# Kernel tuning notes

Hardware: AMD Instinct MI355X
Metric: run time of the kernel (lower is better)

The kernel has to match this reference:

```python
import jax, jax.numpy as jnp
import numpy as np

T, H, I, E, K = 8192, 2048, 768, 16, 2  # tokens, hidden, moe_intermediate, experts, top_k


def setup_inputs() -> dict:
    key = jax.random.key(0)
    k0, k1, k2, k3, k4 = jax.random.split(key, 5)
    return {
        "hidden_states": jax.random.normal(k0, (T, H), jnp.float32),
        "top_k_index": jax.random.randint(k1, (T, K), 0, E),
        "top_k_weights": jax.random.uniform(k2, (T, K), jnp.float32),
        "gate_up_proj": jax.random.normal(k3, (E, 2 * I, H), jnp.float32) * 0.02,
        "down_proj": jax.random.normal(k4, (E, H, I), jnp.float32) * 0.02,
    }


def reference(hidden_states, top_k_index, top_k_weights, gate_up_proj, down_proj):
    num_experts = gate_up_proj.shape[0]
    # combine[t, e] = sum over k of top_k_weights[t, k] where top_k_index[t, k] == e
    # (duplicated expert picks sum their weights, matching torch index_add_ semantics)
    onehot = jax.nn.one_hot(top_k_index, num_experts, dtype=hidden_states.dtype)  # [T, K, E]
    combine = jnp.einsum("tke,tk->te", onehot, top_k_weights)                      # [T, E]
    out = jnp.zeros_like(hidden_states)
    # fixed small loop over structurally distinct experts; unselected tokens get weight 0
    for e in range(num_experts):
        gate_up = hidden_states @ gate_up_proj[e].T        # [T, 2I]
        gate, up = jnp.split(gate_up, 2, axis=-1)
        act = jax.nn.silu(gate) * up                       # SwiGLU, [T, I]
        down = act @ down_proj[e].T                        # [T, H]
        out = out + down * combine[:, e:e + 1]
    return out
```

## Files before the change

### kernel.cpp

```cpp
#include <hip/hip_runtime.h>

#define TT 8192
#define HH 2048
#define II 768
#define NE 16
#define TOPK 2
#define CAP 16384
#define BM 128

typedef float f32x4 __attribute__((ext_vector_type(4)));
typedef short bf16x8 __attribute__((ext_vector_type(8)));
typedef unsigned short ushort8 __attribute__((ext_vector_type(8)));

__device__ __forceinline__ unsigned short f2bf(float f) {
    unsigned u = __builtin_bit_cast(unsigned, f);
    u += 0x7fffu + ((u >> 16) & 1u);
    return (unsigned short)(u >> 16);
}

__device__ __forceinline__ void glds16(const void* g, void* l) {
    __builtin_amdgcn_global_load_lds((const __attribute__((address_space(1))) void*)g,
                                     (__attribute__((address_space(3))) void*)l, 16, 0, 0);
}

__global__ void cast_hs_kernel(const float* __restrict__ src, unsigned short* __restrict__ dst) {
    int i = blockIdx.x * blockDim.x + threadIdx.x;
    const float4 v = reinterpret_cast<const float4*>(src)[i];
    ushort4 o;
    o.x = f2bf(v.x); o.y = f2bf(v.y); o.z = f2bf(v.z); o.w = f2bf(v.w);
    reinterpret_cast<ushort4*>(dst)[i] = o;
}

__global__ void cast_w1_kernel(const float* __restrict__ gup, unsigned short* __restrict__ wg1) {
    size_t gid = (size_t)blockIdx.x * 256 + threadIdx.x;
    int sc = gid & 7;
    int r = (gid >> 3) & 255;
    int kt = (gid >> 11) & 31;
    int rest = (int)(gid >> 16);
    int it = rest % 6;
    int e = rest / 6;
    int chunk = sc ^ (r & 7);
    int grow = (r < 128) ? (it * 128 + r) : (II + it * 128 + (r - 128));
    const float4* s = reinterpret_cast<const float4*>(
        &gup[((size_t)e * (2 * II) + grow) * HH + kt * 64 + chunk * 8]);
    float4 v0 = s[0], v1 = s[1];
    ushort8 o;
    o[0] = f2bf(v0.x); o[1] = f2bf(v0.y); o[2] = f2bf(v0.z); o[3] = f2bf(v0.w);
    o[4] = f2bf(v1.x); o[5] = f2bf(v1.y); o[6] = f2bf(v1.z); o[7] = f2bf(v1.w);
    *reinterpret_cast<ushort8*>(&wg1[gid * 8]) = o;
}

__global__ void cast_w2_kernel(const float* __restrict__ dwn, unsigned short* __restrict__ wg2) {
    size_t gid = (size_t)blockIdx.x * 256 + threadIdx.x;
    int sc = gid & 7;
    int r = (gid >> 3) & 127;
    int kt = (int)((gid >> 10) % 12);
    int rest = (int)(gid / (12 << 10));
    int ht = rest & 15;
    int e = rest >> 4;
    int chunk = sc ^ (r & 7);
    int hrow = ht * 128 + r;
    const float4* s = reinterpret_cast<const float4*>(
        &dwn[((size_t)e * HH + hrow) * II + kt * 64 + chunk * 8]);
    float4 v0 = s[0], v1 = s[1];
    ushort8 o;
    o[0] = f2bf(v0.x); o[1] = f2bf(v0.y); o[2] = f2bf(v0.z); o[3] = f2bf(v0.w);
    o[4] = f2bf(v1.x); o[5] = f2bf(v1.y); o[6] = f2bf(v1.z); o[7] = f2bf(v1.w);
    *reinterpret_cast<ushort8*>(&wg2[gid * 8]) = o;
}

__global__ void route_kernel(const int* __restrict__ idx, const float* __restrict__ w,
                             int* __restrict__ counts, int* __restrict__ toks,
                             float* __restrict__ wts) {
    int t = blockIdx.x * blockDim.x + threadIdx.x;
    if (t >= TT) return;
    #pragma unroll
    for (int k = 0; k < TOPK; ++k) {
        int e = idx[t * TOPK + k];
        int p = atomicAdd(&counts[e], 1);
        toks[e * CAP + p] = t | (k << 15);
        wts[e * CAP + p] = w[t * TOPK + k];
    }
}

__global__ void scan_kernel(const int* __restrict__ counts, int* __restrict__ poffs,
                            int* __restrict__ ntot, int* __restrict__ tmap) {
    if (threadIdx.x == 0) {
        int s = 0, nt = 0;
        for (int e = 0; e < NE; ++e) {
            poffs[e] = s;
            int ct = (counts[e] + 127) >> 7;
            for (int m = 0; m < ct; ++m) tmap[nt++] = e | (m << 8);
            s += ct << 7;
        }
        poffs[NE] = s;
        ntot[0] = nt;
    }
}

__global__ __launch_bounds__(256, 2) void gemm1_kernel(
    const unsigned short* __restrict__ hsb, const unsigned short* __restrict__ wg1,
    const int* __restrict__ counts, const int* __restrict__ poffs,
    const int* __restrict__ ntotp, const int* __restrict__ tmap,
    const int* __restrict__ toks, unsigned short* __restrict__ actT) {
    const int gt = blockIdx.y;
    if (gt >= ntotp[0]) return;
    const int ent = tmap[gt];
    const int e = ent & 255;
    const int mbase = (ent >> 8) << 7;
    const int cnt = counts[e];
    const int ibt = blockIdx.x;
    const int tid = threadIdx.x;
    const int lane = tid & 63;
    const int wid = tid >> 6;
    const int wm = wid >> 1, wn = wid & 1;

    __shared__ unsigned short sA[128 * 64];
    __shared__ unsigned short sB[256 * 64];
    __shared__ int s_tok[BM];

    if (tid < BM) {
        int r = mbase + tid;
        s_tok[tid] = toks[e * CAP + ((r < cnt) ? r : (cnt - 1))] & 0x1FFF;
    }
    __syncthreads();

    size_t abase[4];
    #pragma unroll
    for (int it = 0; it < 4; ++it) {
        int idx = it * 256 + tid;
        int r = idx >> 3, sc = idx & 7;
        abase[it] = (size_t)s_tok[r] * HH + ((sc ^ (r & 7)) << 3);
    }
    const unsigned short* bbase = wg1 + ((size_t)(e * 6 + ibt) << 19) + (size_t)tid * 8;

    f32x4 accg[4][4], accu[4][4];
    #pragma unroll
    for (int m = 0; m < 4; ++m)
        #pragma unroll
        for (int n = 0; n < 4; ++n) {
            accg[m][n] = (f32x4){0.f, 0.f, 0.f, 0.f};
            accu[m][n] = (f32x4){0.f, 0.f, 0.f, 0.f};
        }

    const int lrow = lane & 15;
    const int lk8 = (lane >> 4) << 3;

    for (int k0 = 0; k0 < HH; k0 += 64) {
        #pragma unroll
        for (int it = 0; it < 4; ++it)
            glds16(hsb + abase[it] + k0, (char*)sA + it * 4096 + wid * 1024);
        const unsigned short* bk = bbase + ((size_t)(k0 >> 6) * 16384);
        #pragma unroll
        for (int it = 0; it < 8; ++it)
            glds16(bk + it * 2048, (char*)sB + it * 4096 + wid * 1024);
        __syncthreads();
        #pragma unroll
        for (int ks = 0; ks < 2; ++ks) {
            bf16x8 af[4], bg[4], bu[4];
            #pragma unroll
            for (int m = 0; m < 4; ++m) {
                int row = wm * 64 + m * 16 + lrow;
                af[m] = *reinterpret_cast<const bf16x8*>(
                    &sA[(row << 6) + ((ks * 32 + lk8) ^ ((row & 7) << 3))]);
            }
            #pragma unroll
            for (int n = 0; n < 4; ++n) {
                int rg = wn * 64 + n * 16 + lrow;
                bg[n] = *reinterpret_cast<const bf16x8*>(
                    &sB[(rg << 6) + ((ks * 32 + lk8) ^ ((rg & 7) << 3))]);
                int ru = rg + 128;
                bu[n] = *reinterpret_cast<const bf16x8*>(
                    &sB[(ru << 6) + ((ks * 32 + lk8) ^ ((ru & 7) << 3))]);
            }
            #pragma unroll
            for (int m = 0; m < 4; ++m)
                #pragma unroll
                for (int n = 0; n < 4; ++n) {
                    accg[m][n] = __builtin_amdgcn_mfma_f32_16x16x32_bf16(af[m], bg[n], accg[m][n], 0, 0, 0);
                    accu[m][n] = __builtin_amdgcn_mfma_f32_16x16x32_bf16(af[m], bu[n], accu[m][n], 0, 0, 0);
                }
        }
        __syncthreads();
    }

    const int mt = (poffs[e] + mbase) >> 7;
    #pragma unroll
    for (int m = 0; m < 4; ++m)
        #pragma unroll
        for (int n = 0; n < 4; ++n)
            #pragma unroll
            for (int j = 0; j < 4; ++j) {
                int row = wm * 64 + m * 16 + ((lane >> 4) << 2) + j;
                if (mbase + row < cnt) {
                    int c = wn * 64 + n * 16 + lrow;
                    int ktile = ibt * 2 + (c >> 6);
                    int cc = c & 63;
                    float g = accg[m][n][j], u = accu[m][n][j];
                    float a = (g / (1.f + __expf(-g))) * u;
                    actT[((size_t)(mt * 12 + ktile) * 128 + row) * 64 +
                         (((cc >> 3) ^ (row & 7)) << 3) + (cc & 7)] = f2bf(a);
                }
            }
}

__global__ __launch_bounds__(256) void gemm2_kernel(
    const unsigned short* __restrict__ actT, const unsigned short* __restrict__ wg2,
    const int* __restrict__ counts, const int* __restrict__ poffs,
    const int* __restrict__ ntotp, const int* __restrict__ tmap,
    const int* __restrict__ toks, const float* __restrict__ wts,
    float* __restrict__ partial) {
    const int gt = blockIdx.y;
    if (gt >= ntotp[0]) return;
    const int ent = tmap[gt];
    const int e = ent & 255;
    const int mbase = (ent >> 8) << 7;
    const int cnt = counts[e];
    const int ht = blockIdx.x;
    const int tid = threadIdx.x;
    const int lane = tid & 63;
    const int wid = tid >> 6;
    const int wm = wid >> 1, wn = wid & 1;

    __shared__ unsigned short sA[128 * 64];
    __shared__ unsigned short sB[128 * 64];
    __shared__ int s_tok[BM];
    __shared__ float s_wt[BM];

    if (tid < BM) {
        int r = mbase + tid;
        int rc = (r < cnt) ? r : (cnt - 1);
        s_tok[tid] = toks[e * CAP + rc];
        s_wt[tid] = wts[e * CAP + rc];
    }

    const int mt = (poffs[e] + mbase) >> 7;
    const unsigned short* abase = actT + (size_t)(mt * 12) * 8192 + (size_t)tid * 8;
    const unsigned short* bbase = wg2 + (size_t)((e * 16 + ht) * 12) * 8192 + (size_t)tid * 8;

    f32x4 acc[4][4];
    #pragma unroll
    for (int m = 0; m < 4; ++m)
        #pragma unroll
        for (int n = 0; n < 4; ++n) acc[m][n] = (f32x4){0.f, 0.f, 0.f, 0.f};

    const int lrow = lane & 15;
    const int lk8 = (lane >> 4) << 3;

    for (int kt = 0; kt < 12; ++kt) {
        #pragma unroll
        for (int it = 0; it < 4; ++it)
            glds16(abase + (size_t)kt * 8192 + it * 2048, (char*)sA + it * 4096 + wid * 1024);
        #pragma unroll
        for (int it = 0; it < 4; ++it)
            glds16(bbase + (size_t)kt * 8192 + it * 2048, (char*)sB + it * 4096 + wid * 1024);
        __syncthreads();
        #pragma unroll
        for (int ks = 0; ks < 2; ++ks) {
            bf16x8 af[4], bb[4];
            #pragma unroll
            for (int m = 0; m < 4; ++m) {
                int row = wm * 64 + m * 16 + lrow;
                af[m] = *reinterpret_cast<const bf16x8*>(
                    &sA[(row << 6) + ((ks * 32 + lk8) ^ ((row & 7) << 3))]);
            }
            #pragma unroll
            for (int n = 0; n < 4; ++n) {
                int rb = wn * 64 + n * 16 + lrow;
                bb[n] = *reinterpret_cast<const bf16x8*>(
                    &sB[(rb << 6) + ((ks * 32 + lk8) ^ ((rb & 7) << 3))]);
            }
            #pragma unroll
            for (int m = 0; m < 4; ++m)
                #pragma unroll
                for (int n = 0; n < 4; ++n)
                    acc[m][n] = __builtin_amdgcn_mfma_f32_16x16x32_bf16(af[m], bb[n], acc[m][n], 0, 0, 0);
        }
        __syncthreads();
    }

    #pragma unroll
    for (int m = 0; m < 4; ++m) {
        int row = wm * 64 + m * 16 + ((lane >> 4) << 2);
        #pragma unroll
        for (int j = 0; j < 4; ++j) {
            if (mbase + row + j < cnt) {
                int v = s_tok[row + j];
                size_t rbase = ((size_t)(v >> 15) * TT + (v & 0x1FFF)) * HH + ht * 128;
                float w = s_wt[row + j];
                #pragma unroll
                for (int n = 0; n < 4; ++n)
                    partial[rbase + wn * 64 + n * 16 + lrow] = acc[m][n][j] * w;
            }
        }
    }
}

__global__ void combine_kernel(const float* __restrict__ partial, float* __restrict__ out) {
    int i = blockIdx.x * blockDim.x + threadIdx.x;
    const float4 a = reinterpret_cast<const float4*>(partial)[i];
    const float4 b = reinterpret_cast<const float4*>(partial + (size_t)TT * HH)[i];
    float4 o;
    o.x = a.x + b.x; o.y = a.y + b.y; o.z = a.z + b.z; o.w = a.w + b.w;
    reinterpret_cast<float4*>(out)[i] = o;
}

extern "C" void kernel_launch(void* const* d_in, const int* in_sizes, int n_in,
                              void* d_out, int out_size, void* d_ws, size_t ws_size,
                              hipStream_t stream) {
    const float* hs = (const float*)d_in[0];
    const int* tki = (const int*)d_in[1];
    const float* tkw = (const float*)d_in[2];
    const float* gup = (const float*)d_in[3];
    const float* dwn = (const float*)d_in[4];
    float* out = (float*)d_out;

    char* ws = (char*)d_ws;
    int* counts = (int*)(ws);
    int* poffs = (int*)(ws + 128);
    int* ntot = (int*)(ws + 224);
    int* tmap = (int*)(ws + 256);
    int* toks = (int*)(ws + 1024);
    float* wts = (float*)(ws + 1024 + (size_t)CAP * NE * 4);
    unsigned short* hsb = (unsigned short*)(ws + 2098176);
    unsigned short* wg1 = (unsigned short*)(ws + 35652608);
    unsigned short* wg2 = (unsigned short*)(ws + 136315904);
    unsigned short* actT = (unsigned short*)(ws + 186647552);
    float* partial = (float*)(ws + 2098176);

    hipMemsetAsync(counts, 0, 1024, stream);
    route_kernel<<<TT / 256, 256, 0, stream>>>(tki, tkw, counts, toks, wts);
    scan_kernel<<<1, 64, 0, stream>>>(counts, poffs, ntot, tmap);
    cast_hs_kernel<<<(TT * HH / 4) / 256, 256, 0, stream>>>(hs, hsb);
    cast_w1_kernel<<<24576, 256, 0, stream>>>(gup, wg1);
    cast_w2_kernel<<<12288, 256, 0, stream>>>(dwn, wg2);
    gemm1_kernel<<<dim3(6, 144), 256, 0, stream>>>(hsb, wg1, counts, poffs, ntot, tmap, toks, actT);
    gemm2_kernel<<<dim3(16, 144), 256, 0, stream>>>(actT, wg2, counts, poffs, ntot, tmap, toks, wts, partial);
    combine_kernel<<<(TT * HH / 4) / 256, 256, 0, stream>>>(partial, out);
}
```

Before: 408.3 us.

## Store MoE partials in bf16 and remap GEMM blocks for XCD locality

```diff
diff --git a/kernel.cpp b/kernel.cpp
--- a/kernel.cpp
+++ b/kernel.cpp
@@ -9,6 +9,7 @@
 #define BM 128
 
 typedef float f32x4 __attribute__((ext_vector_type(4)));
+typedef float f32x8 __attribute__((ext_vector_type(8)));
 typedef short bf16x8 __attribute__((ext_vector_type(8)));
 typedef unsigned short ushort8 __attribute__((ext_vector_type(8)));
 
@@ -16,6 +17,10 @@
     unsigned u = __builtin_bit_cast(unsigned, f);
     u += 0x7fffu + ((u >> 16) & 1u);
     return (unsigned short)(u >> 16);
+}
+
+__device__ __forceinline__ float bf2f(unsigned short u) {
+    return __builtin_bit_cast(float, (unsigned)u << 16);
 }
 
 __device__ __forceinline__ void glds16(const void* g, void* l) {
@@ -103,13 +108,15 @@
     const int* __restrict__ counts, const int* __restrict__ poffs,
     const int* __restrict__ ntotp, const int* __restrict__ tmap,
     const int* __restrict__ toks, unsigned short* __restrict__ actT) {
-    const int gt = blockIdx.y;
+    const int b = blockIdx.x;
+    const int w = (b & 7) * 108 + (b >> 3);
+    const int ibt = w / 144;
+    const int gt = w % 144;
     if (gt >= ntotp[0]) return;
     const int ent = tmap[gt];
     const int e = ent & 255;
     const int mbase = (ent >> 8) << 7;
     const int cnt = counts[e];
-    const int ibt = blockIdx.x;
     const int tid = threadIdx.x;
     const int lane = tid & 63;
     const int wid = tid >> 6;
@@ -209,14 +216,16 @@
     const int* __restrict__ counts, const int* __restrict__ poffs,
     const int* __restrict__ ntotp, const int* __restrict__ tmap,
     const int* __restrict__ toks, const float* __restrict__ wts,
-    float* __restrict__ partial) {
-    const int gt = blockIdx.y;
+    unsigned short* __restrict__ partial) {
+    const int b = blockIdx.x;
+    const int w = (b & 7) * 288 + (b >> 3);
+    const int ht = w / 144;
+    const int gt = w % 144;
     if (gt >= ntotp[0]) return;
     const int ent = tmap[gt];
     const int e = ent & 255;
     const int mbase = (ent >> 8) << 7;
     const int cnt = counts[e];
-    const int ht = blockIdx.x;
     const int tid = threadIdx.x;
     const int lane = tid & 63;
     const int wid = tid >> 6;
@@ -290,19 +299,20 @@
                 float w = s_wt[row + j];
                 #pragma unroll
                 for (int n = 0; n < 4; ++n)
-                    partial[rbase + wn * 64 + n * 16 + lrow] = acc[m][n][j] * w;
-            }
-        }
-    }
-}
-
-__global__ void combine_kernel(const float* __restrict__ partial, float* __restrict__ out) {
-    int i = blockIdx.x * blockDim.x + threadIdx.x;
-    const float4 a = reinterpret_cast<const float4*>(partial)[i];
-    const float4 b = reinterpret_cast<const float4*>(partial + (size_t)TT * HH)[i];
-    float4 o;
-    o.x = a.x + b.x; o.y = a.y + b.y; o.z = a.z + b.z; o.w = a.w + b.w;
-    reinterpret_cast<float4*>(out)[i] = o;
+                    partial[rbase + wn * 64 + n * 16 + lrow] = f2bf(acc[m][n][j] * w);
+            }
+        }
+    }
+}
+
+__global__ void combine_kernel(const unsigned short* __restrict__ partial, float* __restrict__ out) {
+    size_t i = (size_t)blockIdx.x * blockDim.x + threadIdx.x;
+    const ushort8 a = reinterpret_cast<const ushort8*>(partial)[i];
+    const ushort8 b = reinterpret_cast<const ushort8*>(partial + (size_t)TT * HH)[i];
+    f32x8 o;
+    #pragma unroll
+    for (int j = 0; j < 8; ++j) o[j] = bf2f(a[j]) + bf2f(b[j]);
+    *reinterpret_cast<f32x8*>(&out[i * 8]) = o;
 }
 
 extern "C" void kernel_launch(void* const* d_in, const int* in_sizes, int n_in,
@@ -326,7 +336,7 @@
     unsigned short* wg1 = (unsigned short*)(ws + 35652608);
     unsigned short* wg2 = (unsigned short*)(ws + 136315904);
     unsigned short* actT = (unsigned short*)(ws + 186647552);
-    float* partial = (float*)(ws + 2098176);
+    unsigned short* partial = (unsigned short*)(ws + 2098176);
 
     hipMemsetAsync(counts, 0, 1024, stream);
     route_kernel<<<TT / 256, 256, 0, stream>>>(tki, tkw, counts, toks, wts);
@@ -334,7 +344,7 @@
     cast_hs_kernel<<<(TT * HH / 4) / 256, 256, 0, stream>>>(hs, hsb);
     cast_w1_kernel<<<24576, 256, 0, stream>>>(gup, wg1);
     cast_w2_kernel<<<12288, 256, 0, stream>>>(dwn, wg2);
-    gemm1_kernel<<<dim3(6, 144), 256, 0, stream>>>(hsb, wg1, counts, poffs, ntot, tmap, toks, actT);
-    gemm2_kernel<<<dim3(16, 144), 256, 0, stream>>>(actT, wg2, counts, poffs, ntot, tmap, toks, wts, partial);
-    combine_kernel<<<(TT * HH / 4) / 256, 256, 0, stream>>>(partial, out);
-}
+    gemm1_kernel<<<864, 256, 0, stream>>>(hsb, wg1, counts, poffs, ntot, tmap, toks, actT);
+    gemm2_kernel<<<2304, 256, 0, stream>>>(actT, wg2, counts, poffs, ntot, tmap, toks, wts, partial);
+    combine_kernel<<<(TT * HH / 8) / 256, 256, 0, stream>>>(partial, out);
+}
```

Measured after the change: 394.5 us. 1.04x faster.
